# Kernel optimization log

Measured on AMD Instinct MI355X. Metric: run time of the kernel, lower is better.

The kernel has to match this reference:

```python
import jax, jax.numpy as jnp
import numpy as np

H = 4096          # hidden_size
NH = 32           # num query heads
NKV = 8           # num kv heads
HD = H // NH      # head_dim = 128
NE = 8            # num_experts
TOPK = 2
ROPE_THETA = 10000.0
EPS = 1e-6


def rmsnorm(x, w):
    var = jnp.mean(x * x, axis=-1, keepdims=True)
    return x * jax.lax.rsqrt(var + EPS) * w


def apply_rope_neox(x, positions):
    # x: [N, heads, HD]; neox style: rotate halves
    half = HD // 2
    inv_freq = 1.0 / (ROPE_THETA ** (jnp.arange(0, HD, 2, dtype=jnp.float32) / HD))  # [half]
    ang = positions.astype(jnp.float32)[:, None] * inv_freq[None, :]                 # [N, half]
    cos = jnp.cos(ang)[:, None, :]  # [N,1,half]
    sin = jnp.sin(ang)[:, None, :]
    x1, x2 = x[..., :half], x[..., half:]
    return jnp.concatenate([x1 * cos - x2 * sin, x2 * cos + x1 * sin], axis=-1)


def setup_inputs() -> dict:
    key = jax.random.key(0)
    ks = jax.random.split(key, 6)
    N = 2048
    return {
        "positions": jnp.arange(N, dtype=jnp.int32),
        "hidden_states": jax.random.normal(ks[0], (N, H), dtype=jnp.float32),
        "w_qkv": jax.random.normal(ks[1], (H, (NH + 2 * NKV) * HD), dtype=jnp.float32) * 0.02,
        "w_o": jax.random.normal(ks[2], (NH * HD, H), dtype=jnp.float32) * 0.02,
        "w_gate": jax.random.normal(ks[3], (H, NE), dtype=jnp.float32) * 0.02,
        "rms_w_pre": jnp.ones((H,), dtype=jnp.float32),
        "rms_w_post": jnp.ones((H,), dtype=jnp.float32),
        "expert_logits": jax.random.uniform(ks[4], (N, NE), dtype=jnp.float32),
    }


def reference(positions, hidden_states, w_qkv, w_o, w_gate, rms_w_pre, rms_w_post, expert_logits):
    N = hidden_states.shape[0]
    # pre-attention RMSNorm (residual is None branch)
    residual = hidden_states
    x = rmsnorm(hidden_states, rms_w_pre)

    qkv = x @ w_qkv
    q = qkv[:, : NH * HD].reshape(N, NH, HD)
    k = qkv[:, NH * HD : (NH + NKV) * HD].reshape(N, NKV, HD)
    v = qkv[:, (NH + NKV) * HD :].reshape(N, NKV, HD)

    q = apply_rope_neox(q, positions)
    k = apply_rope_neox(k, positions)

    # GQA causal self-attention (prefill, single sequence)
    group = NH // NKV
    k_rep = jnp.repeat(k, group, axis=1)  # [N, NH, HD]
    v_rep = jnp.repeat(v, group, axis=1)
    scale = HD ** -0.5
    scores = jnp.einsum("qhd,khd->hqk", q, k_rep) * scale  # [NH, N, N]
    causal = jnp.tril(jnp.ones((N, N), dtype=bool))
    scores = jnp.where(causal[None], scores, jnp.finfo(scores.dtype).min)
    probs = jax.nn.softmax(scores, axis=-1)
    attn_out = jnp.einsum("hqk,khd->qhd", probs, v_rep).reshape(N, NH * HD)

    output = attn_out @ w_o
    # post-attention RMSNorm with fused residual add (vLLM semantics)
    s = output + residual
    residual = s
    output = rmsnorm(s, rms_w_post)

    router_logits = output @ w_gate  # computed as in source; routing result overwritten below

    # random_routing: topk over random expert logits, renormalized
    topk_weights, topk_ids = jax.lax.top_k(expert_logits, TOPK)  # [N, TOPK]
    topk_weights = topk_weights / jnp.sum(topk_weights, axis=-1, keepdims=True)

    # permute_by_exp_ids: stable sort of flattened expert ids, gather tokens
    reorder_ids = jnp.argsort(topk_ids.reshape(-1), stable=True)  # [N*TOPK]
    permuted_output = output[reorder_ids // TOPK]                 # [N*TOPK, H]
    return permuted_output, topk_weights, topk_ids, reorder_ids
```

## Files before the change

kernel.cpp:

```cpp
#include <hip/hip_runtime.h>
#include <hip/hip_bf16.h>
#include <math.h>

#define N_TOK 2048
#define H_DIM 4096
#define NH 32
#define NKV 8
#define HD 128
#define QKV_D 6144
#define NE 8
#define TOPK 2

#define OUT_PERM 0
#define OUT_W    16777216
#define OUT_IDS  16781312
#define OUT_REO  16785408

typedef __bf16 bf16x8 __attribute__((ext_vector_type(8)));
typedef float f32x4 __attribute__((ext_vector_type(4)));

typedef __attribute__((address_space(3))) void lds_void;
typedef __attribute__((address_space(1))) const void gbl_void;

__device__ __forceinline__ void gld16(const void* g, void* l) {
    __builtin_amdgcn_global_load_lds((gbl_void*)g, (lds_void*)l, 16, 0, 0);
}

__device__ __forceinline__ unsigned short f2bf(float f) {
    union { float f; unsigned u; } v; v.f = f;
    unsigned r = v.u + 0x7fff + ((v.u >> 16) & 1);
    return (unsigned short)(r >> 16);
}
__device__ __forceinline__ unsigned pack2bf(float a, float b) {
    return (unsigned)f2bf(a) | ((unsigned)f2bf(b) << 16);
}
__device__ __forceinline__ float bf2f(unsigned short u) {
    union { unsigned u; float f; } v; v.u = ((unsigned)u) << 16;
    return v.f;
}

__global__ __launch_bounds__(256) void rmsnorm_k(const float* __restrict__ x,
                                                 const float* __restrict__ w,
                                                 float* __restrict__ yf,
                                                 unsigned short* __restrict__ yb) {
    int row = blockIdx.x;
    int tid = threadIdx.x;
    const float4* x4 = (const float4*)(x + (size_t)row * H_DIM);
    const float4* w4 = (const float4*)w;
    float4 v[4];
    float ss = 0.f;
#pragma unroll
    for (int k = 0; k < 4; ++k) {
        v[k] = x4[tid + k * 256];
        ss += v[k].x * v[k].x + v[k].y * v[k].y + v[k].z * v[k].z + v[k].w * v[k].w;
    }
#pragma unroll
    for (int off = 32; off; off >>= 1) ss += __shfl_xor(ss, off);
    __shared__ float sacc[4];
    if ((tid & 63) == 0) sacc[tid >> 6] = ss;
    __syncthreads();
    float tot = sacc[0] + sacc[1] + sacc[2] + sacc[3];
    float sc = rsqrtf(tot * (1.0f / H_DIM) + 1e-6f);
#pragma unroll
    for (int k = 0; k < 4; ++k) {
        float4 ww = w4[tid + k * 256];
        float4 o;
        o.x = v[k].x * sc * ww.x;
        o.y = v[k].y * sc * ww.y;
        o.z = v[k].z * sc * ww.z;
        o.w = v[k].w * sc * ww.w;
        if (yf) {
            *(float4*)(yf + (size_t)row * H_DIM + (tid + k * 256) * 4) = o;
        } else {
            uint2 p;
            p.x = pack2bf(o.x, o.y);
            p.y = pack2bf(o.z, o.w);
            *(uint2*)(yb + (size_t)row * H_DIM + (tid + k * 256) * 4) = p;
        }
    }
}

__global__ __launch_bounds__(256) void convT_k(const float* __restrict__ src,
                                               unsigned short* __restrict__ dst,
                                               int R, int C) {
    __shared__ float t[64][68];
    int r0 = blockIdx.y * 64, c0 = blockIdx.x * 64;
    int tid = threadIdx.x;
    int lr = tid >> 4, lc = tid & 15;
#pragma unroll
    for (int it = 0; it < 4; ++it) {
        int r = lr + it * 16;
        float4 v = *(const float4*)(src + (size_t)(r0 + r) * C + c0 + lc * 4);
        *(float4*)&t[r][lc * 4] = v;
    }
    __syncthreads();
#pragma unroll
    for (int it = 0; it < 4; ++it) {
        int cc = lr + it * 16;
        uint2 o;
        o.x = pack2bf(t[lc * 4 + 0][cc], t[lc * 4 + 1][cc]);
        o.y = pack2bf(t[lc * 4 + 2][cc], t[lc * 4 + 3][cc]);
        *(uint2*)(dst + (size_t)(c0 + cc) * R + r0 + lc * 4) = o;
    }
}

__global__ __launch_bounds__(256) void gemm_k(const __hip_bfloat16* __restrict__ A,
                                              const __hip_bfloat16* __restrict__ Bt,
                                              float* __restrict__ C,
                                              unsigned short* __restrict__ Cb,
                                              const float* __restrict__ residual,
                                              int Ncols) {
    __shared__ __align__(16) __hip_bfloat16 As[2][128 * 64];
    __shared__ __align__(16) __hip_bfloat16 Bs[2][128 * 64];
    const int K = H_DIM;
    int tid = threadIdx.x, w = tid >> 6, lane = tid & 63;
    int quad = lane >> 4, l15 = lane & 15;

    int gx = gridDim.x;
    int nwg = gx * gridDim.y;
    int v = blockIdx.y * gx + blockIdx.x;
    int lin = (v & 7) * (nwg >> 3) + (v >> 3);
    int m0 = (lin % gx) * 128, n0 = (lin / gx) * 128;
    int wm = (w & 1) * 64, wn = (w >> 1) * 64;

    int rowInChunk = lane >> 3;
    int uIdx = lane & 7;
    const char* Ag[4]; const char* Bg[4];
    int chOff[4];
#pragma unroll
    for (int c = 0; c < 4; ++c) {
        int ch = w * 4 + c;
        int r = ch * 8 + rowInChunk;
        int gu = uIdx ^ (r & 7);
        Ag[c] = (const char*)(A + (size_t)(m0 + r) * K) + gu * 16;
        Bg[c] = (const char*)(Bt + (size_t)(n0 + r) * K) + gu * 16;
        chOff[c] = ch * 1024;
    }

    f32x4 acc[4][4];
#pragma unroll
    for (int i = 0; i < 4; ++i)
#pragma unroll
        for (int j = 0; j < 4; ++j) acc[i][j] = (f32x4){0.f, 0.f, 0.f, 0.f};

    const int nsteps = K / 64;

#pragma unroll
    for (int c = 0; c < 4; ++c) gld16(Ag[c], (char*)&As[0][0] + chOff[c]);
#pragma unroll
    for (int c = 0; c < 4; ++c) gld16(Bg[c], (char*)&Bs[0][0] + chOff[c]);

    for (int t = 0; t < nsteps; ++t) {
        int cur = t & 1;
        if (t + 1 < nsteps) {
            size_t kb = (size_t)(t + 1) * 128;
            char* dA = (char*)&As[cur ^ 1][0];
            char* dB = (char*)&Bs[cur ^ 1][0];
#pragma unroll
            for (int c = 0; c < 4; ++c) gld16(Ag[c] + kb, dA + chOff[c]);
#pragma unroll
            for (int c = 0; c < 4; ++c) gld16(Bg[c] + kb, dB + chOff[c]);
            asm volatile("s_waitcnt vmcnt(8)" ::: "memory");
        } else {
            asm volatile("s_waitcnt vmcnt(0)" ::: "memory");
        }
        __builtin_amdgcn_sched_barrier(0);
        __builtin_amdgcn_s_barrier();
        __builtin_amdgcn_sched_barrier(0);

        const char* sA = (const char*)&As[cur][0];
        const char* sB = (const char*)&Bs[cur][0];
#pragma unroll
        for (int kk = 0; kk < 2; ++kk) {
            bf16x8 af[4], bfr[4];
#pragma unroll
            for (int mt = 0; mt < 4; ++mt) {
                int m = wm + mt * 16 + l15;
                af[mt] = *(const bf16x8*)(sA + m * 128 + (((kk * 4 + quad) ^ (m & 7)) * 16));
            }
#pragma unroll
            for (int nt = 0; nt < 4; ++nt) {
                int n = wn + nt * 16 + l15;
                bfr[nt] = *(const bf16x8*)(sB + n * 128 + (((kk * 4 + quad) ^ (n & 7)) * 16));
            }
#pragma unroll
            for (int mt = 0; mt < 4; ++mt)
#pragma unroll
                for (int nt = 0; nt < 4; ++nt)
                    acc[mt][nt] = __builtin_amdgcn_mfma_f32_16x16x32_bf16(af[mt], bfr[nt], acc[mt][nt], 0, 0, 0);
        }
        __builtin_amdgcn_sched_barrier(0);
        __builtin_amdgcn_s_barrier();
        __builtin_amdgcn_sched_barrier(0);
    }
#pragma unroll
    for (int mt = 0; mt < 4; ++mt)
#pragma unroll
        for (int nt = 0; nt < 4; ++nt)
#pragma unroll
            for (int r = 0; r < 4; ++r) {
                int row = m0 + wm + mt * 16 + quad * 4 + r;
                int col = n0 + wn + nt * 16 + l15;
                size_t off = (size_t)row * Ncols + col;
                float vv = acc[mt][nt][r];
                if (Cb) {
                    Cb[off] = f2bf(vv);
                } else {
                    if (residual) vv += residual[off];
                    C[off] = vv;
                }
            }
}

__global__ __launch_bounds__(256) void prep_k(const unsigned short* __restrict__ qkvb,
                                              const int* __restrict__ pos,
                                              unsigned short* __restrict__ Qc,
                                              unsigned short* __restrict__ Kc) {
    int row = blockIdx.x, tid = threadIdx.x;
    float fpos = (float)pos[row];
    const float scale = 0.08838834764831845f;
    const float lg = 0.20762050593045f;
#pragma unroll
    for (int it = 0; it < 8; ++it) {
        int pi = tid + it * 256;
        int head = pi >> 6, t = pi & 63;
        float inv = exp2f(-(float)t * lg);
        float ang = fpos * inv;
        float s = __sinf(ang), c = __cosf(ang);
        const unsigned short* bp = qkvb + (size_t)row * QKV_D + head * HD + t;
        float x1 = bf2f(bp[0]), x2 = bf2f(bp[64]);
        unsigned short* qb = Qc + (size_t)row * H_DIM + head * HD + t;
        qb[0]  = f2bf((x1 * c - x2 * s) * scale);
        qb[64] = f2bf((x2 * c + x1 * s) * scale);
    }
#pragma unroll
    for (int it = 0; it < 2; ++it) {
        int pi = tid + it * 256;
        int kvh = pi >> 6, t = pi & 63;
        float inv = exp2f(-(float)t * lg);
        float ang = fpos * inv;
        float s = __sinf(ang), c = __cosf(ang);
        const unsigned short* bp = qkvb + (size_t)row * QKV_D + H_DIM + kvh * HD + t;
        float x1 = bf2f(bp[0]), x2 = bf2f(bp[64]);
        unsigned short* kb = Kc + ((size_t)kvh * N_TOK + row) * HD + t;
        kb[0]  = f2bf(x1 * c - x2 * s);
        kb[64] = f2bf(x2 * c + x1 * s);
    }
}

__global__ __launch_bounds__(256) void vt_k(const unsigned short* __restrict__ qkvb,
                                            unsigned short* __restrict__ Vt) {
    __shared__ unsigned short ts[64][136];
    int j0 = blockIdx.x * 64, kvh = blockIdx.y, tid = threadIdx.x;
#pragma unroll
    for (int it = 0; it < 4; ++it) {
        int idx = tid + it * 256;
        int r = idx >> 4, c8 = idx & 15;
        *(uint4*)&ts[r][c8 * 8] =
            *(const uint4*)(qkvb + (size_t)(j0 + r) * QKV_D + (NH + NKV) * HD + kvh * HD + c8 * 8);
    }
    __syncthreads();
    int d = tid >> 1, half = tid & 1;
    unsigned short* dst = Vt + ((size_t)kvh * HD + d) * N_TOK + j0 + half * 32;
#pragma unroll
    for (int g = 0; g < 4; ++g) {
        int kb = half * 32 + g * 8;
        uint4 o;
        o.x = (unsigned)ts[kb + 0][d] | ((unsigned)ts[kb + 1][d] << 16);
        o.y = (unsigned)ts[kb + 2][d] | ((unsigned)ts[kb + 3][d] << 16);
        o.z = (unsigned)ts[kb + 4][d] | ((unsigned)ts[kb + 5][d] << 16);
        o.w = (unsigned)ts[kb + 6][d] | ((unsigned)ts[kb + 7][d] << 16);
        *(uint4*)(dst + g * 8) = o;
    }
}

__global__ __launch_bounds__(512) void attn_k(const __hip_bfloat16* __restrict__ Qc,
                                              const __hip_bfloat16* __restrict__ Kc,
                                              const __hip_bfloat16* __restrict__ Vt,
                                              unsigned short* __restrict__ ao) {
    __shared__ __align__(16) __hip_bfloat16 Ks[2][32 * 128];
    __shared__ __align__(16) __hip_bfloat16 Vs[2][128 * 32];
    __shared__ __align__(16) unsigned short Pw[8][16 * 40];

    int tid = threadIdx.x, w = tid >> 6, lane = tid & 63;
    int quad = lane >> 4, l15 = lane & 15;
    int pr = blockIdx.y;
    int kvh = pr >> 1;
    int h = kvh * 4 + (pr & 1) * 2 + (w & 1);
    int qt = gridDim.x - 1 - blockIdx.x;
    int i0 = qt * 64;
    int i0q = i0 + (w >> 1) * 16;
    int q = i0q + l15;

    bf16x8 qf[4];
    const __hip_bfloat16* qrow = Qc + (size_t)q * H_DIM + h * HD;
#pragma unroll
    for (int kf = 0; kf < 4; ++kf)
        qf[kf] = *(const bf16x8*)(qrow + kf * 32 + quad * 8);

    const char* KcH = (const char*)(Kc + (size_t)kvh * N_TOK * HD);
    const char* VtH = (const char*)(Vt + (size_t)kvh * HD * N_TOK);

    int kKey = w * 4 + (lane >> 4);
    int kPart = (lane & 15) ^ (kKey & 15);
    int vD = w * 16 + (lane >> 2);
    int vP = (lane & 3) ^ (vD & 3);
    char* Kl[2] = { (char*)&Ks[0][0] + w * 1024, (char*)&Ks[1][0] + w * 1024 };
    char* Vl[2] = { (char*)&Vs[0][0] + w * 1024, (char*)&Vs[1][0] + w * 1024 };

    float mstat = -INFINITY, lstat = 0.f;
    f32x4 o[8];
#pragma unroll
    for (int nt = 0; nt < 8; ++nt) o[nt] = (f32x4){0.f, 0.f, 0.f, 0.f};

    int nsteps = (i0 + 64) >> 5;

    gld16(KcH + (size_t)kKey * 256 + kPart * 16, Kl[0]);
    gld16(VtH + (size_t)vD * (N_TOK * 2) + vP * 16, Vl[0]);
    __syncthreads();

    for (int t = 0; t < nsteps; ++t) {
        int j0 = t << 5;
        int cur = t & 1;
        if (t + 1 < nsteps) {
            int jn = j0 + 32;
            gld16(KcH + (size_t)(jn + kKey) * 256 + kPart * 16, Kl[cur ^ 1]);
            gld16(VtH + (size_t)vD * (N_TOK * 2) + (size_t)jn * 2 + vP * 16, Vl[cur ^ 1]);
        }
        if (j0 <= i0q + 15) {
            const char* Kb = (const char*)&Ks[cur][0];
            const char* Vb = (const char*)&Vs[cur][0];

            f32x4 s[2];
            s[0] = (f32x4){0.f, 0.f, 0.f, 0.f};
            s[1] = (f32x4){0.f, 0.f, 0.f, 0.f};
#pragma unroll
            for (int mt = 0; mt < 2; ++mt) {
                int key = mt * 16 + l15;
#pragma unroll
                for (int kf = 0; kf < 4; ++kf) {
                    bf16x8 kfr = *(const bf16x8*)(Kb + key * 256 + (((kf * 4 + quad) ^ (key & 15)) * 16));
                    s[mt] = __builtin_amdgcn_mfma_f32_16x16x32_bf16(kfr, qf[kf], s[mt], 0, 0, 0);
                }
            }
            if (j0 + 31 > i0q) {
#pragma unroll
                for (int mt = 0; mt < 2; ++mt) {
                    int keyb = j0 + mt * 16 + quad * 4;
#pragma unroll
                    for (int r = 0; r < 4; ++r)
                        if (keyb + r > q) s[mt][r] = -INFINITY;
                }
            }
            float mx = fmaxf(fmaxf(fmaxf(s[0][0], s[0][1]), fmaxf(s[0][2], s[0][3])),
                             fmaxf(fmaxf(s[1][0], s[1][1]), fmaxf(s[1][2], s[1][3])));
            mx = fmaxf(mx, __shfl_xor(mx, 16));
            mx = fmaxf(mx, __shfl_xor(mx, 32));
            float newm = fmaxf(mstat, mx);
            float alpha = __expf(mstat - newm);
            float p[8];
#pragma unroll
            for (int mt = 0; mt < 2; ++mt)
#pragma unroll
                for (int r = 0; r < 4; ++r) p[mt * 4 + r] = __expf(s[mt][r] - newm);
            float ps = p[0] + p[1] + p[2] + p[3] + p[4] + p[5] + p[6] + p[7];
            ps += __shfl_xor(ps, 16);
            ps += __shfl_xor(ps, 32);
            lstat = lstat * alpha + ps;
            mstat = newm;

            unsigned* pwb = (unsigned*)(&Pw[w][0]);
            int eo = l15 * 20 + quad * 2;
            pwb[eo]     = pack2bf(p[0], p[1]);
            pwb[eo + 1] = pack2bf(p[2], p[3]);
            pwb[eo + 8] = pack2bf(p[4], p[5]);
            pwb[eo + 9] = pack2bf(p[6], p[7]);
            bf16x8 pf = *(const bf16x8*)(&Pw[w][l15 * 40 + quad * 8]);

            float alq[4];
#pragma unroll
            for (int r = 0; r < 4; ++r) alq[r] = __shfl(alpha, quad * 4 + r);
#pragma unroll
            for (int nt = 0; nt < 8; ++nt)
#pragma unroll
                for (int r = 0; r < 4; ++r) o[nt][r] *= alq[r];

#pragma unroll
            for (int nt = 0; nt < 8; ++nt) {
                int d = nt * 16 + l15;
                bf16x8 vf = *(const bf16x8*)(Vb + d * 64 + ((quad ^ (d & 3)) * 16));
                o[nt] = __builtin_amdgcn_mfma_f32_16x16x32_bf16(pf, vf, o[nt], 0, 0, 0);
            }
        }
        __syncthreads();
    }

    float linv[4];
#pragma unroll
    for (int r = 0; r < 4; ++r) linv[r] = 1.f / __shfl(lstat, quad * 4 + r);
#pragma unroll
    for (int nt = 0; nt < 8; ++nt)
#pragma unroll
        for (int r = 0; r < 4; ++r) {
            int row = i0q + quad * 4 + r;
            int col = h * HD + nt * 16 + l15;
            ao[(size_t)row * H_DIM + col] = f2bf(o[nt][r] * linv[r]);
        }
}

__global__ __launch_bounds__(256) void topk_k(const float* __restrict__ elog,
                                              float* __restrict__ w_out,
                                              float* __restrict__ id_out,
                                              int* __restrict__ ids_int) {
    int row = blockIdx.x * 256 + threadIdx.x;
    if (row >= N_TOK) return;
    const float4* e4 = (const float4*)(elog + (size_t)row * NE);
    float4 a = e4[0], b = e4[1];
    float e[8] = {a.x, a.y, a.z, a.w, b.x, b.y, b.z, b.w};
    int id0 = 0;
    float b0 = e[0];
#pragma unroll
    for (int t = 1; t < 8; ++t)
        if (e[t] > b0) { b0 = e[t]; id0 = t; }
    int id1 = -1;
    float b1 = -INFINITY;
#pragma unroll
    for (int t = 0; t < 8; ++t)
        if (t != id0 && e[t] > b1) { b1 = e[t]; id1 = t; }
    float s = b0 + b1;
    w_out[row * 2 + 0] = b0 / s;
    w_out[row * 2 + 1] = b1 / s;
    id_out[row * 2 + 0] = (float)id0;
    id_out[row * 2 + 1] = (float)id1;
    ids_int[row * 2 + 0] = id0;
    ids_int[row * 2 + 1] = id1;
}

__global__ __launch_bounds__(256) void sort_k(const int* __restrict__ ids,
                                              float* __restrict__ reorder_out,
                                              int* __restrict__ perm) {
    __shared__ int sh[N_TOK * TOPK];
    int tid = threadIdx.x;
    for (int r = tid; r < N_TOK * TOPK; r += 256) sh[r] = ids[r];
    __syncthreads();
    int i = blockIdx.x * 256 + tid;
    int e = sh[i];
    int rank = 0;
    for (int j = 0; j < N_TOK * TOPK; ++j) {
        int ej = sh[j];
        rank += (ej < e) ? 1 : ((ej == e && j < i) ? 1 : 0);
    }
    reorder_out[rank] = (float)i;
    perm[rank] = i;
}

__global__ __launch_bounds__(256) void gather_k(const float* __restrict__ src,
                                                const int* __restrict__ perm,
                                                float* __restrict__ dst) {
    int r = blockIdx.x;
    int srow = perm[r] >> 1;
    const float4* s4 = (const float4*)(src + (size_t)srow * H_DIM);
    float4* d4 = (float4*)(dst + (size_t)r * H_DIM);
    int tid = threadIdx.x;
#pragma unroll
    for (int k = 0; k < 4; ++k) d4[tid + k * 256] = s4[tid + k * 256];
}

extern "C" void kernel_launch(void* const* d_in, const int* in_sizes, int n_in,
                              void* d_out, int out_size, void* d_ws, size_t ws_size,
                              hipStream_t stream) {
    const int*   positions = (const int*)d_in[0];
    const float* hidden    = (const float*)d_in[1];
    const float* w_qkv     = (const float*)d_in[2];
    const float* w_o       = (const float*)d_in[3];
    const float* rms_pre   = (const float*)d_in[5];
    const float* rms_post  = (const float*)d_in[6];
    const float* elog      = (const float*)d_in[7];
    float* out = (float*)d_out;

    char* ws = (char*)d_ws;
    unsigned short* wqkvT = (unsigned short*)(ws);
    unsigned short* woT   = (unsigned short*)(ws);
    float*          post  = (float*)(ws + 33554432ULL);
    unsigned short* xn    = (unsigned short*)(ws + 50331648ULL);
    unsigned short* aout  = (unsigned short*)(ws + 50331648ULL);
    unsigned short* qkvb  = (unsigned short*)(ws + 67108864ULL);
    float*          sbuf  = (float*)(ws + 67108864ULL);
    unsigned short* Qc    = (unsigned short*)(ws + 117440512ULL);
    unsigned short* Kc    = (unsigned short*)(ws + 134217728ULL);
    unsigned short* Vt    = (unsigned short*)(ws + 138412032ULL);
    int* ids_int  = (int*)(ws + 142606336ULL);
    int* perm_int = (int*)(ws + 142622720ULL);

    convT_k<<<dim3(QKV_D / 64, H_DIM / 64), 256, 0, stream>>>(w_qkv, wqkvT, H_DIM, QKV_D);
    rmsnorm_k<<<N_TOK, 256, 0, stream>>>(hidden, rms_pre, nullptr, xn);
    gemm_k<<<dim3(N_TOK / 128, QKV_D / 128), 256, 0, stream>>>(
        (const __hip_bfloat16*)xn, (const __hip_bfloat16*)wqkvT, nullptr, qkvb, nullptr, QKV_D);
    convT_k<<<dim3(H_DIM / 64, H_DIM / 64), 256, 0, stream>>>(w_o, woT, H_DIM, H_DIM);
    prep_k<<<N_TOK, 256, 0, stream>>>(qkvb, positions, Qc, Kc);
    vt_k<<<dim3(N_TOK / 64, NKV), 256, 0, stream>>>(qkvb, Vt);
    attn_k<<<dim3(N_TOK / 64, 16), 512, 0, stream>>>(
        (const __hip_bfloat16*)Qc, (const __hip_bfloat16*)Kc, (const __hip_bfloat16*)Vt, aout);
    gemm_k<<<dim3(N_TOK / 128, H_DIM / 128), 256, 0, stream>>>(
        (const __hip_bfloat16*)aout, (const __hip_bfloat16*)woT, sbuf, nullptr, hidden, H_DIM);
    rmsnorm_k<<<N_TOK, 256, 0, stream>>>(sbuf, rms_post, post, nullptr);
    topk_k<<<N_TOK / 256, 256, 0, stream>>>(elog, out + OUT_W, out + OUT_IDS, ids_int);
    sort_k<<<(N_TOK * TOPK) / 256, 256, 0, stream>>>(ids_int, out + OUT_REO, perm_int);
    gather_k<<<N_TOK * TOPK, 256, 0, stream>>>(post, perm_int, out + OUT_PERM);
}
```

Measured before the change: 735.3 us.

## Use 256x256 eight-wave pipelined GEMM for the QKV projection

```diff
diff --git a/kernel.cpp b/kernel.cpp
--- a/kernel.cpp
+++ b/kernel.cpp
@@ -212,6 +212,182 @@
             }
 }
 
+__global__ __launch_bounds__(512) void gemm8_k(const __hip_bfloat16* __restrict__ A,
+                                               const __hip_bfloat16* __restrict__ Bt,
+                                               unsigned short* __restrict__ Cb,
+                                               int Ncols) {
+    __shared__ __align__(16) __hip_bfloat16 As[2][256 * 64];
+    __shared__ __align__(16) __hip_bfloat16 Bs[2][256 * 64];
+    const int K = H_DIM;
+    int tid = threadIdx.x, w = tid >> 6, lane = tid & 63;
+    int quad = lane >> 4, l15 = lane & 15;
+    int wr = w >> 2, wc = w & 3;
+
+    int gx = gridDim.x;
+    int nwg = gx * gridDim.y;
+    int v = blockIdx.y * gx + blockIdx.x;
+    int lin = (v & 7) * (nwg >> 3) + (v >> 3);
+    int m0 = (lin % gx) * 256, n0 = (lin / gx) * 256;
+
+    const char* Abase = (const char*)A + (size_t)m0 * (K * 2);
+    const char* Bbase = (const char*)Bt + (size_t)n0 * (K * 2);
+    int srow = w * 8 + (lane >> 3);
+
+    auto stage = [&](const char* gbase, int rowoff, char* lbase, size_t kbyte) {
+#pragma unroll
+        for (int l = 0; l < 2; ++l) {
+            int r = l * 64 + srow;
+            int gu = (lane & 7) ^ (r & 7);
+            gld16(gbase + (size_t)(rowoff + r) * (K * 2) + kbyte + gu * 16,
+                  lbase + (l * 64 + w * 8) * 128);
+        }
+    };
+
+    f32x4 acc[8][4];
+#pragma unroll
+    for (int i = 0; i < 8; ++i)
+#pragma unroll
+        for (int j = 0; j < 4; ++j) acc[i][j] = (f32x4){0.f, 0.f, 0.f, 0.f};
+
+    const int ntiles = K / 64;
+
+    stage(Abase, 0,   (char*)&As[0][0],         0);
+    stage(Abase, 128, (char*)&As[0][0] + 16384, 0);
+    stage(Bbase, 0,   (char*)&Bs[0][0],         0);
+    stage(Bbase, 128, (char*)&Bs[0][0] + 16384, 0);
+    stage(Bbase, 0,   (char*)&Bs[1][0],         128);
+    stage(Bbase, 128, (char*)&Bs[1][0] + 16384, 128);
+    asm volatile("s_waitcnt vmcnt(4)" ::: "memory");
+    __builtin_amdgcn_sched_barrier(0);
+    __builtin_amdgcn_s_barrier();
+    __builtin_amdgcn_sched_barrier(0);
+
+    for (int j = 0; j < ntiles; ++j) {
+        int d = j & 1;
+        const char* sA = (const char*)&As[d][0];
+        const char* sB = (const char*)&Bs[d][0];
+        char* nA = (char*)&As[d ^ 1][0];
+        char* pB = (char*)&Bs[d][0];
+        size_t kb1 = (size_t)(j + 1) * 128, kb2 = (size_t)(j + 2) * 128;
+        bf16x8 aR[4][2], bR[4][2];
+
+#pragma unroll
+        for (int mt = 0; mt < 4; ++mt)
+#pragma unroll
+            for (int kk = 0; kk < 2; ++kk) {
+                int m = wr * 128 + mt * 16 + l15;
+                aR[mt][kk] = *(const bf16x8*)(sA + m * 128 + (((kk * 4 + quad) ^ (m & 7)) * 16));
+            }
+#pragma unroll
+        for (int nt = 0; nt < 2; ++nt)
+#pragma unroll
+            for (int kk = 0; kk < 2; ++kk) {
+                int n = wc * 64 + nt * 16 + l15;
+                bR[nt][kk] = *(const bf16x8*)(sB + n * 128 + (((kk * 4 + quad) ^ (n & 7)) * 16));
+            }
+        if (j + 1 < ntiles) stage(Abase, 0, nA, kb1);
+        __builtin_amdgcn_sched_barrier(0);
+        __builtin_amdgcn_s_barrier();
+        asm volatile("s_waitcnt lgkmcnt(0)" ::: "memory");
+        __builtin_amdgcn_sched_barrier(0);
+        __builtin_amdgcn_s_setprio(1);
+#pragma unroll
+        for (int mt = 0; mt < 4; ++mt)
+#pragma unroll
+            for (int nt = 0; nt < 2; ++nt)
+#pragma unroll
+                for (int kk = 0; kk < 2; ++kk)
+                    acc[mt][nt] = __builtin_amdgcn_mfma_f32_16x16x32_bf16(aR[mt][kk], bR[nt][kk], acc[mt][nt], 0, 0, 0);
+        __builtin_amdgcn_s_setprio(0);
+        __builtin_amdgcn_sched_barrier(0);
+        __builtin_amdgcn_s_barrier();
+        __builtin_amdgcn_sched_barrier(0);
+
+#pragma unroll
+        for (int nt = 2; nt < 4; ++nt)
+#pragma unroll
+            for (int kk = 0; kk < 2; ++kk) {
+                int n = wc * 64 + nt * 16 + l15;
+                bR[nt][kk] = *(const bf16x8*)(sB + n * 128 + (((kk * 4 + quad) ^ (n & 7)) * 16));
+            }
+        if (j + 1 < ntiles) stage(Abase, 128, nA + 16384, kb1);
+        __builtin_amdgcn_sched_barrier(0);
+        __builtin_amdgcn_s_barrier();
+        asm volatile("s_waitcnt lgkmcnt(0)" ::: "memory");
+        __builtin_amdgcn_sched_barrier(0);
+        __builtin_amdgcn_s_setprio(1);
+#pragma unroll
+        for (int mt = 0; mt < 4; ++mt)
+#pragma unroll
+            for (int nt = 2; nt < 4; ++nt)
+#pragma unroll
+                for (int kk = 0; kk < 2; ++kk)
+                    acc[mt][nt] = __builtin_amdgcn_mfma_f32_16x16x32_bf16(aR[mt][kk], bR[nt][kk], acc[mt][nt], 0, 0, 0);
+        __builtin_amdgcn_s_setprio(0);
+        __builtin_amdgcn_sched_barrier(0);
+        __builtin_amdgcn_s_barrier();
+        __builtin_amdgcn_sched_barrier(0);
+
+#pragma unroll
+        for (int mt = 0; mt < 4; ++mt)
+#pragma unroll
+            for (int kk = 0; kk < 2; ++kk) {
+                int m = wr * 128 + (mt + 4) * 16 + l15;
+                aR[mt][kk] = *(const bf16x8*)(sA + m * 128 + (((kk * 4 + quad) ^ (m & 7)) * 16));
+            }
+        if (j + 2 < ntiles) stage(Bbase, 0, pB, kb2);
+        __builtin_amdgcn_sched_barrier(0);
+        __builtin_amdgcn_s_barrier();
+        asm volatile("s_waitcnt lgkmcnt(0)" ::: "memory");
+        __builtin_amdgcn_sched_barrier(0);
+        __builtin_amdgcn_s_setprio(1);
+#pragma unroll
+        for (int mt = 0; mt < 4; ++mt)
+#pragma unroll
+            for (int nt = 0; nt < 2; ++nt)
+#pragma unroll
+                for (int kk = 0; kk < 2; ++kk)
+                    acc[mt + 4][nt] = __builtin_amdgcn_mfma_f32_16x16x32_bf16(aR[mt][kk], bR[nt][kk], acc[mt + 4][nt], 0, 0, 0);
+        __builtin_amdgcn_s_setprio(0);
+        __builtin_amdgcn_sched_barrier(0);
+        __builtin_amdgcn_s_barrier();
+        __builtin_amdgcn_sched_barrier(0);
+
+        if (j + 2 < ntiles) {
+            stage(Bbase, 128, pB + 16384, kb2);
+            asm volatile("s_waitcnt vmcnt(4)" ::: "memory");
+        } else {
+            asm volatile("s_waitcnt vmcnt(0)" ::: "memory");
+        }
+        __builtin_amdgcn_sched_barrier(0);
+        __builtin_amdgcn_s_barrier();
+        __builtin_amdgcn_sched_barrier(0);
+        __builtin_amdgcn_s_setprio(1);
+#pragma unroll
+        for (int mt = 0; mt < 4; ++mt)
+#pragma unroll
+            for (int nt = 2; nt < 4; ++nt)
+#pragma unroll
+                for (int kk = 0; kk < 2; ++kk)
+                    acc[mt + 4][nt] = __builtin_amdgcn_mfma_f32_16x16x32_bf16(aR[mt][kk], bR[nt][kk], acc[mt + 4][nt], 0, 0, 0);
+        __builtin_amdgcn_s_setprio(0);
+        __builtin_amdgcn_sched_barrier(0);
+        __builtin_amdgcn_s_barrier();
+        __builtin_amdgcn_sched_barrier(0);
+    }
+
+#pragma unroll
+    for (int mt = 0; mt < 8; ++mt)
+#pragma unroll
+        for (int nt = 0; nt < 4; ++nt)
+#pragma unroll
+            for (int r = 0; r < 4; ++r) {
+                int row = m0 + wr * 128 + mt * 16 + quad * 4 + r;
+                int col = n0 + wc * 64 + nt * 16 + l15;
+                Cb[(size_t)row * Ncols + col] = f2bf(acc[mt][nt][r]);
+            }
+}
+
 __global__ __launch_bounds__(256) void prep_k(const unsigned short* __restrict__ qkvb,
                                               const int* __restrict__ pos,
                                               unsigned short* __restrict__ Qc,
@@ -494,8 +670,8 @@
 
     convT_k<<<dim3(QKV_D / 64, H_DIM / 64), 256, 0, stream>>>(w_qkv, wqkvT, H_DIM, QKV_D);
     rmsnorm_k<<<N_TOK, 256, 0, stream>>>(hidden, rms_pre, nullptr, xn);
-    gemm_k<<<dim3(N_TOK / 128, QKV_D / 128), 256, 0, stream>>>(
-        (const __hip_bfloat16*)xn, (const __hip_bfloat16*)wqkvT, nullptr, qkvb, nullptr, QKV_D);
+    gemm8_k<<<dim3(N_TOK / 256, QKV_D / 256), 512, 0, stream>>>(
+        (const __hip_bfloat16*)xn, (const __hip_bfloat16*)wqkvT, qkvb, QKV_D);
     convT_k<<<dim3(H_DIM / 64, H_DIM / 64), 256, 0, stream>>>(w_o, woT, H_DIM, H_DIM);
     prep_k<<<N_TOK, 256, 0, stream>>>(qkvb, positions, Qc, Kc);
     vt_k<<<dim3(N_TOK / 64, NKV), 256, 0, stream>>>(qkvb, Vt);
```

New measurement: 717.3 us. 2.4% less time.

## Replace 128x128 GEMM with 256-row tiled 8-wave GEMM with staggered prefetch

Applied to the files above, without the earlier changes.

```diff
diff --git a/kernel.cpp b/kernel.cpp
--- a/kernel.cpp
+++ b/kernel.cpp
@@ -104,108 +104,143 @@
     }
 }
 
-__global__ __launch_bounds__(256) void gemm_k(const __hip_bfloat16* __restrict__ A,
-                                              const __hip_bfloat16* __restrict__ Bt,
-                                              float* __restrict__ C,
-                                              unsigned short* __restrict__ Cb,
-                                              const float* __restrict__ residual,
-                                              int Ncols) {
-    __shared__ __align__(16) __hip_bfloat16 As[2][128 * 64];
-    __shared__ __align__(16) __hip_bfloat16 Bs[2][128 * 64];
+template<int BN, bool BF16OUT>
+__global__ __launch_bounds__(512) void gemm256_k(const __hip_bfloat16* __restrict__ A,
+                                                 const __hip_bfloat16* __restrict__ Bt,
+                                                 float* __restrict__ C,
+                                                 unsigned short* __restrict__ Cb,
+                                                 const float* __restrict__ residual,
+                                                 int Ncols) {
+    constexpr int NT = BN / 64;
+    __shared__ __align__(16) __hip_bfloat16 As[2][256 * 64];
+    __shared__ __align__(16) __hip_bfloat16 Bs[2][BN * 64];
     const int K = H_DIM;
     int tid = threadIdx.x, w = tid >> 6, lane = tid & 63;
     int quad = lane >> 4, l15 = lane & 15;
+    int wr = w >> 2, wc = w & 3;
 
     int gx = gridDim.x;
     int nwg = gx * gridDim.y;
     int v = blockIdx.y * gx + blockIdx.x;
     int lin = (v & 7) * (nwg >> 3) + (v >> 3);
-    int m0 = (lin % gx) * 128, n0 = (lin / gx) * 128;
-    int wm = (w & 1) * 64, wn = (w >> 1) * 64;
-
-    int rowInChunk = lane >> 3;
-    int uIdx = lane & 7;
-    const char* Ag[4]; const char* Bg[4];
-    int chOff[4];
-#pragma unroll
-    for (int c = 0; c < 4; ++c) {
-        int ch = w * 4 + c;
-        int r = ch * 8 + rowInChunk;
-        int gu = uIdx ^ (r & 7);
-        Ag[c] = (const char*)(A + (size_t)(m0 + r) * K) + gu * 16;
-        Bg[c] = (const char*)(Bt + (size_t)(n0 + r) * K) + gu * 16;
-        chOff[c] = ch * 1024;
-    }
-
-    f32x4 acc[4][4];
-#pragma unroll
-    for (int i = 0; i < 4; ++i)
-#pragma unroll
-        for (int j = 0; j < 4; ++j) acc[i][j] = (f32x4){0.f, 0.f, 0.f, 0.f};
-
-    const int nsteps = K / 64;
-
-#pragma unroll
-    for (int c = 0; c < 4; ++c) gld16(Ag[c], (char*)&As[0][0] + chOff[c]);
-#pragma unroll
-    for (int c = 0; c < 4; ++c) gld16(Bg[c], (char*)&Bs[0][0] + chOff[c]);
-
-    for (int t = 0; t < nsteps; ++t) {
-        int cur = t & 1;
-        if (t + 1 < nsteps) {
-            size_t kb = (size_t)(t + 1) * 128;
-            char* dA = (char*)&As[cur ^ 1][0];
-            char* dB = (char*)&Bs[cur ^ 1][0];
-#pragma unroll
-            for (int c = 0; c < 4; ++c) gld16(Ag[c] + kb, dA + chOff[c]);
-#pragma unroll
-            for (int c = 0; c < 4; ++c) gld16(Bg[c] + kb, dB + chOff[c]);
-            asm volatile("s_waitcnt vmcnt(8)" ::: "memory");
-        } else {
-            asm volatile("s_waitcnt vmcnt(0)" ::: "memory");
-        }
+    int m0 = (lin % gx) * 256, n0 = (lin / gx) * BN;
+
+    const char* Abase = (const char*)A + (size_t)m0 * (K * 2);
+    const char* Bbase = (const char*)Bt + (size_t)n0 * (K * 2);
+    int srow = w * 8 + (lane >> 3);
+
+    auto stageA = [&](char* lbase, size_t kbyte) {
+#pragma unroll
+        for (int l = 0; l < 4; ++l) {
+            int r = l * 64 + srow;
+            int gu = (lane & 7) ^ (r & 7);
+            gld16(Abase + (size_t)r * (K * 2) + kbyte + gu * 16,
+                  lbase + (size_t)(l * 64 + w * 8) * 128);
+        }
+    };
+    auto stageB = [&](char* lbase, size_t kbyte) {
+#pragma unroll
+        for (int l = 0; l < NT; ++l) {
+            int r = l * 64 + srow;
+            int gu = (lane & 7) ^ (r & 7);
+            gld16(Bbase + (size_t)r * (K * 2) + kbyte + gu * 16,
+                  lbase + (size_t)(l * 64 + w * 8) * 128);
+        }
+    };
+
+    f32x4 acc[8][NT];
+#pragma unroll
+    for (int i = 0; i < 8; ++i)
+#pragma unroll
+        for (int j = 0; j < NT; ++j) acc[i][j] = (f32x4){0.f, 0.f, 0.f, 0.f};
+
+    const int ntiles = K / 64;
+
+    stageA((char*)&As[0][0], 0);
+    stageB((char*)&Bs[0][0], 0);
+    stageB((char*)&Bs[1][0], 128);
+    if constexpr (NT == 3) asm volatile("s_waitcnt vmcnt(3)" ::: "memory");
+    else                   asm volatile("s_waitcnt vmcnt(2)" ::: "memory");
+    __builtin_amdgcn_sched_barrier(0);
+    __builtin_amdgcn_s_barrier();
+    __builtin_amdgcn_sched_barrier(0);
+
+    for (int j = 0; j < ntiles; ++j) {
+        int d = j & 1;
+        const char* sA = (const char*)&As[d][0];
+        const char* sB = (const char*)&Bs[d][0];
+        size_t kb1 = (size_t)(j + 1) * 128, kb2 = (size_t)(j + 2) * 128;
+        bf16x8 aR[4][2], bR[NT][2];
+
+#pragma unroll
+        for (int mt = 0; mt < 4; ++mt)
+#pragma unroll
+            for (int kk = 0; kk < 2; ++kk) {
+                int m = wr * 128 + mt * 16 + l15;
+                aR[mt][kk] = *(const bf16x8*)(sA + m * 128 + (((kk * 4 + quad) ^ (m & 7)) * 16));
+            }
+#pragma unroll
+        for (int nt = 0; nt < NT; ++nt)
+#pragma unroll
+            for (int kk = 0; kk < 2; ++kk) {
+                int n = wc * (NT * 16) + nt * 16 + l15;
+                bR[nt][kk] = *(const bf16x8*)(sB + n * 128 + (((kk * 4 + quad) ^ (n & 7)) * 16));
+            }
+        if (j + 1 < ntiles) stageA((char*)&As[d ^ 1][0], kb1);
+        __builtin_amdgcn_s_setprio(1);
+#pragma unroll
+        for (int mt = 0; mt < 4; ++mt)
+#pragma unroll
+            for (int nt = 0; nt < NT; ++nt)
+#pragma unroll
+                for (int kk = 0; kk < 2; ++kk)
+                    acc[mt][nt] = __builtin_amdgcn_mfma_f32_16x16x32_bf16(aR[mt][kk], bR[nt][kk], acc[mt][nt], 0, 0, 0);
+        __builtin_amdgcn_s_setprio(0);
         __builtin_amdgcn_sched_barrier(0);
         __builtin_amdgcn_s_barrier();
         __builtin_amdgcn_sched_barrier(0);
 
-        const char* sA = (const char*)&As[cur][0];
-        const char* sB = (const char*)&Bs[cur][0];
-#pragma unroll
-        for (int kk = 0; kk < 2; ++kk) {
-            bf16x8 af[4], bfr[4];
-#pragma unroll
-            for (int mt = 0; mt < 4; ++mt) {
-                int m = wm + mt * 16 + l15;
-                af[mt] = *(const bf16x8*)(sA + m * 128 + (((kk * 4 + quad) ^ (m & 7)) * 16));
-            }
-#pragma unroll
-            for (int nt = 0; nt < 4; ++nt) {
-                int n = wn + nt * 16 + l15;
-                bfr[nt] = *(const bf16x8*)(sB + n * 128 + (((kk * 4 + quad) ^ (n & 7)) * 16));
-            }
-#pragma unroll
-            for (int mt = 0; mt < 4; ++mt)
-#pragma unroll
-                for (int nt = 0; nt < 4; ++nt)
-                    acc[mt][nt] = __builtin_amdgcn_mfma_f32_16x16x32_bf16(af[mt], bfr[nt], acc[mt][nt], 0, 0, 0);
+#pragma unroll
+        for (int mt = 0; mt < 4; ++mt)
+#pragma unroll
+            for (int kk = 0; kk < 2; ++kk) {
+                int m = wr * 128 + (mt + 4) * 16 + l15;
+                aR[mt][kk] = *(const bf16x8*)(sA + m * 128 + (((kk * 4 + quad) ^ (m & 7)) * 16));
+            }
+        if (j + 2 < ntiles) stageB((char*)&Bs[d][0], kb2);
+        __builtin_amdgcn_s_setprio(1);
+#pragma unroll
+        for (int mt = 0; mt < 4; ++mt)
+#pragma unroll
+            for (int nt = 0; nt < NT; ++nt)
+#pragma unroll
+                for (int kk = 0; kk < 2; ++kk)
+                    acc[mt + 4][nt] = __builtin_amdgcn_mfma_f32_16x16x32_bf16(aR[mt][kk], bR[nt][kk], acc[mt + 4][nt], 0, 0, 0);
+        __builtin_amdgcn_s_setprio(0);
+        if (j + 2 < ntiles) {
+            if constexpr (NT == 3) asm volatile("s_waitcnt vmcnt(3)" ::: "memory");
+            else                   asm volatile("s_waitcnt vmcnt(2)" ::: "memory");
+        } else {
+            asm volatile("s_waitcnt vmcnt(0)" ::: "memory");
         }
         __builtin_amdgcn_sched_barrier(0);
         __builtin_amdgcn_s_barrier();
         __builtin_amdgcn_sched_barrier(0);
     }
-#pragma unroll
-    for (int mt = 0; mt < 4; ++mt)
-#pragma unroll
-        for (int nt = 0; nt < 4; ++nt)
+
+#pragma unroll
+    for (int mt = 0; mt < 8; ++mt)
+#pragma unroll
+        for (int nt = 0; nt < NT; ++nt)
 #pragma unroll
             for (int r = 0; r < 4; ++r) {
-                int row = m0 + wm + mt * 16 + quad * 4 + r;
-                int col = n0 + wn + nt * 16 + l15;
+                int row = m0 + wr * 128 + mt * 16 + quad * 4 + r;
+                int col = n0 + wc * (NT * 16) + nt * 16 + l15;
                 size_t off = (size_t)row * Ncols + col;
-                float vv = acc[mt][nt][r];
-                if (Cb) {
-                    Cb[off] = f2bf(vv);
+                if constexpr (BF16OUT) {
+                    Cb[off] = f2bf(acc[mt][nt][r]);
                 } else {
+                    float vv = acc[mt][nt][r];
                     if (residual) vv += residual[off];
                     C[off] = vv;
                 }
@@ -494,14 +529,14 @@
 
     convT_k<<<dim3(QKV_D / 64, H_DIM / 64), 256, 0, stream>>>(w_qkv, wqkvT, H_DIM, QKV_D);
     rmsnorm_k<<<N_TOK, 256, 0, stream>>>(hidden, rms_pre, nullptr, xn);
-    gemm_k<<<dim3(N_TOK / 128, QKV_D / 128), 256, 0, stream>>>(
+    gemm256_k<192, true><<<dim3(N_TOK / 256, QKV_D / 192), 512, 0, stream>>>(
         (const __hip_bfloat16*)xn, (const __hip_bfloat16*)wqkvT, nullptr, qkvb, nullptr, QKV_D);
     convT_k<<<dim3(H_DIM / 64, H_DIM / 64), 256, 0, stream>>>(w_o, woT, H_DIM, H_DIM);
     prep_k<<<N_TOK, 256, 0, stream>>>(qkvb, positions, Qc, Kc);
     vt_k<<<dim3(N_TOK / 64, NKV), 256, 0, stream>>>(qkvb, Vt);
     attn_k<<<dim3(N_TOK / 64, 16), 512, 0, stream>>>(
         (const __hip_bfloat16*)Qc, (const __hip_bfloat16*)Kc, (const __hip_bfloat16*)Vt, aout);
-    gemm_k<<<dim3(N_TOK / 128, H_DIM / 128), 256, 0, stream>>>(
+    gemm256_k<128, false><<<dim3(N_TOK / 256, H_DIM / 128), 512, 0, stream>>>(
         (const __hip_bfloat16*)aout, (const __hip_bfloat16*)woT, sbuf, nullptr, hidden, H_DIM);
     rmsnorm_k<<<N_TOK, 256, 0, stream>>>(sbuf, rms_post, post, nullptr);
     topk_k<<<N_TOK / 256, 256, 0, stream>>>(elog, out + OUT_W, out + OUT_IDS, ids_int);
```

Measured after the change: 668.6 us. 9.1% less time.
